# Optimization experiments

Hardware: AMD Instinct MI355X
Metric: run time of the kernel (lower is better)

Reference implementation:

```python
import math
import jax
import jax.numpy as jnp
import numpy as np

B = 64          # graphs per batch
NPG = 1000      # nodes per graph
IN = 64         # input feature dim
H = 128         # hidden dim
DEG = 16        # avg degree
C = 10          # num classes
RATIO = 0.8     # topk ratio
EPS = 1e-5      # batchnorm eps
E = B * NPG * DEG


def setup_inputs() -> dict:
    key = jax.random.key(0)
    ks = jax.random.split(key, 16)
    x = jax.random.normal(ks[0], (B * NPG, IN), jnp.float32)
    # per-graph random edges, then offset to global node ids
    src = jax.random.randint(ks[1], (B, NPG * DEG), 0, NPG)
    dst = jax.random.randint(ks[2], (B, NPG * DEG), 0, NPG)
    off = (jnp.arange(B) * NPG)[:, None]
    edge_index = jnp.stack([(src + off).reshape(-1), (dst + off).reshape(-1)]).astype(jnp.int32)
    batch = jnp.repeat(jnp.arange(B), NPG).astype(jnp.int32)
    edge_weight = jax.random.uniform(ks[3], (E,), jnp.float32)
    # parameters: block 1 conv is [IN,H]; blocks 2-6 are [H,H] (stacked)
    conv1_w = jax.random.normal(ks[4], (IN, H), jnp.float32) * 0.05
    conv_w = jax.random.normal(ks[5], (5, H, H), jnp.float32) * 0.05
    conv_b = jnp.zeros((6, H), jnp.float32)
    bn_gamma = jnp.ones((6, H), jnp.float32)
    bn_beta = jnp.zeros((6, H), jnp.float32)
    bn_mean = jax.random.normal(ks[6], (6, H), jnp.float32) * 0.01
    bn_var = jax.random.uniform(ks[7], (6, H), jnp.float32, 0.5, 1.5)
    pool_w = jax.random.normal(ks[8], (6, H), jnp.float32)
    d1_w = jax.random.normal(ks[9], (2 * H, 4 * H), jnp.float32) * 0.05
    d1_b = jnp.zeros((4 * H,), jnp.float32)
    d2_w = jax.random.normal(ks[10], (4 * H, C), jnp.float32) * 0.05
    d2_b = jnp.zeros((C,), jnp.float32)
    return dict(x=x, edge_index=edge_index, batch=batch, edge_weight=edge_weight,
                conv1_w=conv1_w, conv_w=conv_w, conv_b=conv_b,
                bn_gamma=bn_gamma, bn_beta=bn_beta, bn_mean=bn_mean, bn_var=bn_var,
                pool_w=pool_w, d1_w=d1_w, d1_b=d1_b, d2_w=d2_w, d2_b=d2_b)


def _gcn_conv(h, src, dst, w_e, W, b, n_nodes):
    # PyG GCNConv: add self-loops (weight 1), sym-normalize, aggregate at dst
    xw = h @ W                                        # [N, H]
    deg = jnp.zeros((n_nodes,), h.dtype).at[dst].add(w_e) + 1.0
    dinv = jax.lax.rsqrt(deg)
    coef = dinv[src] * dinv[dst] * w_e                # [E]
    out = jnp.zeros_like(xw).at[dst].add(coef[:, None] * xw[src])
    out = out + (dinv * dinv)[:, None] * xw + b       # self-loop term + bias
    return out


def reference(x, edge_index, batch, edge_weight, conv1_w, conv_w, conv_b,
              bn_gamma, bn_beta, bn_mean, bn_var, pool_w, d1_w, d1_b, d2_w, d2_b):
    src, dst = edge_index[0], edge_index[1]
    w_e = edge_weight
    h = x
    n_cur = NPG
    flats = jnp.zeros((B, 2 * H), x.dtype)
    for i in range(6):
        N = B * n_cur
        W = conv1_w if i == 0 else conv_w[i - 1]
        hc = _gcn_conv(h, src, dst, w_e, W, conv_b[i], N)
        # BatchNorm (inference) + ReLU
        hc = (hc - bn_mean[i]) * (bn_gamma[i] * jax.lax.rsqrt(bn_var[i] + EPS)) + bn_beta[i]
        hc = jax.nn.relu(hc)
        # TopKPooling: score = tanh(x.w/||w||), keep top ceil(ratio*n) per graph
        pw = pool_w[i]
        score = jnp.tanh(hc @ pw / jnp.linalg.norm(pw))   # [N]
        k = math.ceil(RATIO * n_cur)
        vals, idx = jax.lax.top_k(score.reshape(B, n_cur), k)  # [B,k]
        perm = (idx + (jnp.arange(B) * n_cur)[:, None]).reshape(-1)
        h = hc[perm] * vals.reshape(-1, 1)                # [B*k, H]
        # remap/filter edges; dead edges become (0,0) with weight 0
        inv = jnp.full((N,), -1, jnp.int32).at[perm].set(jnp.arange(B * k, dtype=jnp.int32))
        ok = (inv[src] >= 0) & (inv[dst] >= 0)
        src = jnp.where(ok, inv[src], 0)
        dst = jnp.where(ok, inv[dst], 0)
        w_e = jnp.where(ok, w_e, 0.0)
        n_cur = k
        hb = h.reshape(B, k, H)
        flats = flats + jnp.concatenate([hb.mean(axis=1), hb.max(axis=1)], axis=-1)
    # MLP head (dropout is identity in eval)
    hd = jax.nn.relu(flats @ d1_w + d1_b)
    return hd @ d2_w + d2_b
```

## Files before the change

### kernel.cpp

```cpp
#include <hip/hip_runtime.h>
#include <float.h>
#include <math.h>

#define NGR 64
#define NPG0 1000
#define HDIM 128
#define EG 16000
#define NE (NGR*EG)
#define RPS 1008
#define BNEPS 1e-5f
#define POOL_NB 16

typedef short short8 __attribute__((ext_vector_type(8)));
typedef float f4v __attribute__((ext_vector_type(4)));

__global__ __launch_bounds__(256) void k_wsplit(const float* __restrict__ c1w,
    const float* __restrict__ cw, const float* __restrict__ pw,
    unsigned short* __restrict__ wh, unsigned short* __restrict__ wl,
    float* __restrict__ invnorm){
  int l = blockIdx.x, t = threadIdx.x;
  __shared__ float red[2];
  if(t < 128){
    float v = pw[l*HDIM + t];
    float s = v*v;
    #pragma unroll
    for(int o=32;o>0;o>>=1) s += __shfl_down(s, o, 64);
    if((t & 63)==0) red[t>>6] = s;
  }
  __syncthreads();
  if(t==0) invnorm[l] = 1.0f / sqrtf(red[0]+red[1]);
  int K  = (l==0) ? 64 : 128;
  int sh = (l==0) ? 6 : 7;
  const float* src = (l==0) ? c1w : (cw + (size_t)(l-1)*16384);
  int tot = 128*K;
  for(int o=t;o<tot;o+=256){
    int c = o >> sh, k = o & (K-1);
    float f = src[k*128 + c];
    unsigned u  = __float_as_uint(f);
    unsigned uh = (u + 0x7fffu + ((u>>16)&1u)) & 0xffff0000u;
    float r = f - __uint_as_float(uh);
    unsigned v = __float_as_uint(r);
    int o2 = (k>>3)*1024 + c*8 + (k&7);
    wh[(size_t)l*16384 + o2] = (unsigned short)(uh>>16);
    wl[(size_t)l*16384 + o2] = (unsigned short)((v + 0x7fffu + ((v>>16)&1u))>>16);
  }
}

__global__ __launch_bounds__(256) void k_count0(const int* __restrict__ dst,
    const float* __restrict__ we, int* __restrict__ pcnt, float* __restrict__ pdeg){
  int g = blockIdx.x >> 2, sub = blockIdx.x & 3, t = threadIdx.x;
  __shared__ int   cnt[NPG0];
  __shared__ float degl[NPG0];
  for(int i=t;i<NPG0;i+=256){ cnt[i]=0; degl[i]=0.f; }
  __syncthreads();
  int base = g*EG + sub*4000;
  for(int idx=t; idx<4000; idx+=256){
    int e = base + idx;
    int ld = dst[e] - g*NPG0;
    atomicAdd(&cnt[ld], 1);
    atomicAdd(&degl[ld], we[e]);
  }
  __syncthreads();
  int p = blockIdx.x * NPG0;
  for(int i=t;i<NPG0;i+=256){ pcnt[p+i] = cnt[i]; pdeg[p+i] = degl[i]; }
}

__global__ __launch_bounds__(1024) void k_build(const int* __restrict__ pcnt,
    const float* __restrict__ pdeg, const int* __restrict__ src,
    const int* __restrict__ dst, const float* __restrict__ we,
    int* __restrict__ rp, float* __restrict__ dinvz, float* __restrict__ gsc,
    long long* __restrict__ ec){
  int g = blockIdx.x, t = threadIdx.x;
  __shared__ int sc[2][1024];
  __shared__ int cur[NPG0];
  int c = 0;
  if(t < NPG0){
    c = pcnt[(g*4+0)*NPG0+t] + pcnt[(g*4+1)*NPG0+t]
      + pcnt[(g*4+2)*NPG0+t] + pcnt[(g*4+3)*NPG0+t];
    float dg = pdeg[(g*4+0)*NPG0+t] + pdeg[(g*4+1)*NPG0+t]
             + pdeg[(g*4+2)*NPG0+t] + pdeg[(g*4+3)*NPG0+t];
    float dv = 1.0f / sqrtf(dg + 1.0f);
    dinvz[g*NPG0+t] = dv;
    gsc[g*NPG0+t]   = dv;
  }
  sc[0][t] = c;
  __syncthreads();
  int buf = 0;
  for(int d=1; d<1024; d<<=1){
    int v = sc[buf][t];
    if(t>=d) v += sc[buf][t-d];
    sc[buf^1][t] = v;
    __syncthreads();
    buf ^= 1;
  }
  if(t<=NPG0) rp[g*RPS+t] = (t==0) ? 0 : sc[buf][t-1];
  if(t<NPG0)  cur[t]      = (t==0) ? 0 : sc[buf][t-1];
  __syncthreads();
  int base = g*EG;
  for(int idx=t; idx<EG; idx+=1024){
    int e = base + idx;
    int ld = dst[e] - g*NPG0;
    int pos = atomicAdd(&cur[ld], 1);
    ec[(size_t)base + pos] = (((long long)__float_as_int(we[e]))<<32) | (unsigned)src[e];
  }
}

__device__ inline void bfsplit(float f, unsigned short &h, unsigned short &l){
  unsigned u  = __float_as_uint(f);
  unsigned uh = (u + 0x7fffu + ((u>>16)&1u)) & 0xffff0000u;
  float r = f - __uint_as_float(uh);
  unsigned v = __float_as_uint(r);
  h = (unsigned short)(uh>>16);
  l = (unsigned short)((v + 0x7fffu + ((v>>16)&1u))>>16);
}

template<int KIN>
__global__ __launch_bounds__(256) void k_fused(const int* __restrict__ olist,
    const int* __restrict__ rp, const long long* __restrict__ ec,
    const float* __restrict__ dinvz, const float* __restrict__ gsc,
    const float* __restrict__ h,
    const unsigned short* __restrict__ Wh, const unsigned short* __restrict__ Wl,
    const float* __restrict__ bias, const float* __restrict__ gamma,
    const float* __restrict__ beta, const float* __restrict__ mean,
    const float* __restrict__ var, const float* __restrict__ pw,
    const float* __restrict__ invn_p, float* __restrict__ hout,
    float* __restrict__ score){
  constexpr int L0 = (KIN==64);
  __shared__ __attribute__((aligned(16))) unsigned short AsH[32*KIN];
  __shared__ __attribute__((aligned(16))) unsigned short AsL[32*KIN];
  __shared__ float sp[32][2];
  int t = threadIdx.x;
  int nb = gridDim.x, b = blockIdx.x;
  int q = nb >> 3, r = nb & 7;
  int xcd = b & 7, off = b >> 3;
  int tile = (xcd < r) ? (xcd*(q+1) + off) : (r*(q+1) + (xcd-r)*q + off);
  int r0 = tile * 32;
  const int lane = t & 63, wid = t >> 6;
  const int wr = wid >> 1, wc = wid & 1;
  const int qw = lane >> 4, sl16 = lane & 15;

  for(int rr=0; rr<8; rr++){
    int local = wid*8 + rr;
    int row = r0 + local;
    int d = L0 ? row : olist[row];
    int g = d / NPG0;
    int ld = d - g*NPG0;
    int e0 = rp[g*RPS+ld], e1 = rp[g*RPS+ld+1];
    float dvd = dinvz[d];
    float gsd = gsc[d];
    float4 a0; a0.x=0.f; a0.y=0.f; a0.z=0.f; a0.w=0.f;
    float4 a1; a1.x=0.f; a1.y=0.f; a1.z=0.f; a1.w=0.f;
    for(int b2=e0;b2<e1;b2+=64){
      int mm = e1-b2; if(mm>64) mm=64;
      long long rec = (lane<mm) ? ec[(size_t)g*EG + b2 + lane] : 0;
      int   sl = (int)(rec & 0xffffffffLL);
      float cl = __int_as_float((int)(rec>>32)) * gsc[sl];
      long long pk = (((long long)__float_as_int(cl))<<32) | (unsigned)sl;
      int mr = (mm+15) & ~15;
      for(int jj=0;jj<mr;jj+=16){
        #pragma unroll
        for(int u=0;u<4;u++){
          long long p = __shfl(pk, jj + 4*u + qw, 64);
          float c = __int_as_float((int)(p>>32));
          if(c != 0.f){
            int s = (int)(p & 0xffffffffLL);
            if(L0){
              float4 hv = *(const float4*)(h + (size_t)s*64 + 4*sl16);
              a0.x += c*hv.x; a0.y += c*hv.y; a0.z += c*hv.z; a0.w += c*hv.w;
            } else {
              const float4* hp = (const float4*)(h + (size_t)s*HDIM + 8*sl16);
              float4 h0 = hp[0], h1 = hp[1];
              a0.x += c*h0.x; a0.y += c*h0.y; a0.z += c*h0.z; a0.w += c*h0.w;
              a1.x += c*h1.x; a1.y += c*h1.y; a1.z += c*h1.z; a1.w += c*h1.w;
            }
          }
        }
      }
    }
    a0.x += __shfl_xor(a0.x, 16, 64); a0.y += __shfl_xor(a0.y, 16, 64);
    a0.z += __shfl_xor(a0.z, 16, 64); a0.w += __shfl_xor(a0.w, 16, 64);
    a0.x += __shfl_xor(a0.x, 32, 64); a0.y += __shfl_xor(a0.y, 32, 64);
    a0.z += __shfl_xor(a0.z, 32, 64); a0.w += __shfl_xor(a0.w, 32, 64);
    if(!L0){
      a1.x += __shfl_xor(a1.x, 16, 64); a1.y += __shfl_xor(a1.y, 16, 64);
      a1.z += __shfl_xor(a1.z, 16, 64); a1.w += __shfl_xor(a1.w, 16, 64);
      a1.x += __shfl_xor(a1.x, 32, 64); a1.y += __shfl_xor(a1.y, 32, 64);
      a1.z += __shfl_xor(a1.z, 32, 64); a1.w += __shfl_xor(a1.w, 32, 64);
    }
    if(qw==0){
      if(L0){
        float4 hs = *(const float4*)(h + (size_t)d*64 + 4*sl16);
        float4 o;
        o.x = dvd*(a0.x + gsd*hs.x); o.y = dvd*(a0.y + gsd*hs.y);
        o.z = dvd*(a0.z + gsd*hs.z); o.w = dvd*(a0.w + gsd*hs.w);
        ushort4 h4, l4;
        bfsplit(o.x, h4.x, l4.x); bfsplit(o.y, h4.y, l4.y);
        bfsplit(o.z, h4.z, l4.z); bfsplit(o.w, h4.w, l4.w);
        int off2 = (local*128 + sl16*8) ^ ((local&7)<<4);
        *(ushort4*)((char*)AsH + off2) = h4;
        *(ushort4*)((char*)AsL + off2) = l4;
      } else {
        const float4* hp = (const float4*)(h + (size_t)d*HDIM + 8*sl16);
        float4 s0 = hp[0], s1 = hp[1];
        float4 o0, o1;
        o0.x = dvd*(a0.x + gsd*s0.x); o0.y = dvd*(a0.y + gsd*s0.y);
        o0.z = dvd*(a0.z + gsd*s0.z); o0.w = dvd*(a0.w + gsd*s0.w);
        o1.x = dvd*(a1.x + gsd*s1.x); o1.y = dvd*(a1.y + gsd*s1.y);
        o1.z = dvd*(a1.z + gsd*s1.z); o1.w = dvd*(a1.w + gsd*s1.w);
        ushort4 h4, l4;
        int off2 = (local*256 + sl16*16) ^ ((local&7)<<4);
        bfsplit(o0.x, h4.x, l4.x); bfsplit(o0.y, h4.y, l4.y);
        bfsplit(o0.z, h4.z, l4.z); bfsplit(o0.w, h4.w, l4.w);
        *(ushort4*)((char*)AsH + off2) = h4;
        *(ushort4*)((char*)AsL + off2) = l4;
        bfsplit(o1.x, h4.x, l4.x); bfsplit(o1.y, h4.y, l4.y);
        bfsplit(o1.z, h4.z, l4.z); bfsplit(o1.w, h4.w, l4.w);
        *(ushort4*)((char*)AsH + off2 + 8) = h4;
        *(ushort4*)((char*)AsL + off2 + 8) = l4;
      }
    }
  }
  __syncthreads();

  f4v acc[4];
  #pragma unroll
  for(int n=0;n<4;n++){ acc[n][0]=0.f; acc[n][1]=0.f; acc[n][2]=0.f; acc[n][3]=0.f; }
  #pragma unroll
  for(int ks=0; ks<KIN/32; ks++){
    short8 ah, al, bh[4], bl[4];
    int kb = ks*64 + qw*16;
    int panel = ks*4 + qw;
    #pragma unroll
    for(int n=0;n<4;n++){
      int col = wc*64 + n*16 + sl16;
      int goff = (panel*128 + col)*8;
      bh[n] = *(const short8*)(Wh + goff);
      bl[n] = *(const short8*)(Wl + goff);
    }
    {
      int row = wr*16 + sl16;
      int off2 = (row*(KIN*2) + kb) ^ ((row&7)<<4);
      ah = *(const short8*)((const char*)AsH + off2);
      al = *(const short8*)((const char*)AsL + off2);
    }
    #pragma unroll
    for(int n=0;n<4;n++){
      acc[n] = __builtin_amdgcn_mfma_f32_16x16x32_bf16(ah, bh[n], acc[n], 0,0,0);
      acc[n] = __builtin_amdgcn_mfma_f32_16x16x32_bf16(ah, bl[n], acc[n], 0,0,0);
      acc[n] = __builtin_amdgcn_mfma_f32_16x16x32_bf16(al, bh[n], acc[n], 0,0,0);
      acc[n] = __builtin_amdgcn_mfma_f32_16x16x32_bf16(al, bl[n], acc[n], 0,0,0);
    }
  }

  float invn = invn_p[0];
  float bi[4], scv[4], bt[4], mn[4], pv[4];
  #pragma unroll
  for(int n=0;n<4;n++){
    int c = wc*64 + n*16 + sl16;
    bi[n]  = bias[c];
    scv[n] = gamma[c] * (1.0f/sqrtf(var[c] + BNEPS));
    bt[n]  = beta[c];
    mn[n]  = mean[c];
    pv[n]  = pw[c];
  }
  #pragma unroll
  for(int i=0;i<4;i++){
    int rl  = wr*16 + qw*4 + i;
    int row = r0 + rl;
    int orig = olist ? olist[row] : row;
    float p = 0.f;
    #pragma unroll
    for(int n=0;n<4;n++){
      float v = fmaxf((acc[n][i] + bi[n] - mn[n])*scv[n] + bt[n], 0.f);
      hout[(size_t)orig*HDIM + wc*64 + n*16 + sl16] = v;
      p += v*pv[n];
    }
    p += __shfl_xor(p, 1, 64); p += __shfl_xor(p, 2, 64);
    p += __shfl_xor(p, 4, 64); p += __shfl_xor(p, 8, 64);
    if(sl16==0) sp[rl][wc] = p;
  }
  __syncthreads();
  if(t < 32) score[r0 + t] = tanhf((sp[t][0] + sp[t][1]) * invn);
}

__global__ __launch_bounds__(512) void k_topk(int n, int k,
    const float* __restrict__ score, const int* __restrict__ curlist,
    float* __restrict__ vals, int* __restrict__ nextlist,
    float* __restrict__ dinvz, float* __restrict__ gsc){
  int g = blockIdx.x, t = threadIdx.x;
  __shared__ unsigned keys[1024];
  __shared__ int hist[256];
  __shared__ int ssum[256];
  __shared__ int sc2[2][512];
  __shared__ int eqbuf[1024];
  __shared__ int eqn;
  __shared__ int sh_B, sh_need, sh_E, sh_cut;
  __shared__ unsigned sh_pref;
  for(int i=t;i<n;i+=512){
    unsigned b = __float_as_uint(score[g*n+i]);
    keys[i] = (b & 0x80000000u) ? ~b : (b | 0x80000000u);
  }
  if(t==0){ sh_need = k; sh_pref = 0u; sh_cut = 0x7fffffff; }
  __syncthreads();
  for(int pass=0; pass<4; pass++){
    int shift = 24 - 8*pass;
    if(t<256) hist[t]=0;
    __syncthreads();
    unsigned pref = sh_pref; int need = sh_need;
    for(int i=t;i<n;i+=512){
      unsigned u = keys[i];
      bool m = (pass==0) || ((u >> (shift+8)) == pref);
      if(m) atomicAdd(&hist[(u>>shift)&255], 1);
    }
    __syncthreads();
    if(t<256) ssum[t] = hist[t];
    __syncthreads();
    for(int d=1; d<256; d<<=1){
      int v=0;
      if(t<256) v = ssum[t] + ((t+d<256)? ssum[t+d] : 0);
      __syncthreads();
      if(t<256) ssum[t] = v;
      __syncthreads();
    }
    if(t<256){
      int Sgt = ssum[t] - hist[t];
      if(Sgt < need && need <= ssum[t]) sh_B = t;
    }
    __syncthreads();
    int B = sh_B;
    if(t==0){
      sh_need = need - (ssum[B] - hist[B]);
      sh_pref = (pass==0) ? (unsigned)B : ((pref<<8) | (unsigned)B);
      if(pass==3) sh_E = hist[B];
    }
    __syncthreads();
  }
  unsigned T = sh_pref; int r_eq = sh_need; int E = sh_E;
  if(E > r_eq){
    if(t==0) eqn = 0;
    __syncthreads();
    for(int i=t;i<n;i+=512) if(keys[i]==T){ int p=atomicAdd(&eqn,1); eqbuf[p]=i; }
    __syncthreads();
    if(t==0){
      int last = -1;
      for(int j=0;j<r_eq;j++){
        int mn = 0x7fffffff;
        for(int q=0;q<E;q++){ int v=eqbuf[q]; if(v>last && v<mn) mn=v; }
        last = mn;
      }
      sh_cut = last;
    }
    __syncthreads();
  }
  int cut = sh_cut;
  int c0=0, c1=0;
  {
    int i=t;
    if(i<n){ unsigned u=keys[i]; c0 = (u>T) || (u==T && i<=cut); }
    i=t+512;
    if(i<n){ unsigned u=keys[i]; c1 = (u>T) || (u==T && i<=cut); }
  }
  sc2[0][t] = c0+c1;
  __syncthreads();
  int buf=0;
  for(int d=1; d<512; d<<=1){
    int v = sc2[buf][t];
    if(t>=d) v += sc2[buf][t-d];
    sc2[buf^1][t]=v;
    __syncthreads();
    buf^=1;
  }
  int base = (t==0) ? 0 : sc2[buf][t-1];
  {
    int i=t;
    if(i<n){
      int orig = curlist ? curlist[g*n+i] : (g*NPG0 + i);
      if(c0){
        unsigned u=keys[i];
        float f = __uint_as_float((u & 0x80000000u) ? (u ^ 0x80000000u) : ~u);
        vals[g*k+base]=f; nextlist[g*k+base]=orig; base++;
      } else { dinvz[orig]=0.f; gsc[orig]=0.f; }
    }
    i=t+512;
    if(i<n){
      int orig = curlist ? curlist[g*n+i] : (g*NPG0 + i);
      if(c1){
        unsigned u=keys[i];
        float f = __uint_as_float((u & 0x80000000u) ? (u ^ 0x80000000u) : ~u);
        vals[g*k+base]=f; nextlist[g*k+base]=orig;
      } else { dinvz[orig]=0.f; gsc[orig]=0.f; }
    }
  }
}

__global__ __launch_bounds__(256) void k_gpd(int k, int do_deg,
    const float* __restrict__ hraw, const float* __restrict__ vals,
    const int* __restrict__ nextlist,
    float* __restrict__ sumst, float* __restrict__ maxst,
    const int* __restrict__ rp, const long long* __restrict__ ec,
    float* __restrict__ dinvz, float* __restrict__ gsc){
  int g = blockIdx.x & 63;
  int chunk = blockIdx.x >> 6;
  int wid = threadIdx.x >> 6, lane = threadIdx.x & 63;
  int ww = chunk*4 + wid;
  const int half = lane >> 5, sl32 = lane & 31;
  const int qw   = lane >> 4, sl16 = lane & 15;
  const int NH = POOL_NB*4*2;
  float4 psum; psum.x=0.f; psum.y=0.f; psum.z=0.f; psum.w=0.f;
  float4 pmax; pmax.x=-FLT_MAX; pmax.y=-FLT_MAX; pmax.z=-FLT_MAX; pmax.w=-FLT_MAX;
  for(int j = ww*2 + half; j < k; j += NH){
    float v = vals[g*k+j];
    int d = nextlist[g*k+j];
    float4 hv = *(const float4*)(hraw + (size_t)d*HDIM + 4*sl32);
    float4 o; o.x=hv.x*v; o.y=hv.y*v; o.z=hv.z*v; o.w=hv.w*v;
    psum.x+=o.x; psum.y+=o.y; psum.z+=o.z; psum.w+=o.w;
    pmax.x=fmaxf(pmax.x,o.x); pmax.y=fmaxf(pmax.y,o.y);
    pmax.z=fmaxf(pmax.z,o.z); pmax.w=fmaxf(pmax.w,o.w);
  }
  if(do_deg){
    const int NQ = POOL_NB*4*4;
    for(int j = ww*4 + qw; j < k; j += NQ){
      int d  = nextlist[g*k + j];
      int ld = d - g*NPG0;
      int e0 = rp[g*RPS+ld], e1 = rp[g*RPS+ld+1];
      float deg = 0.f;
      for(int b=e0+sl16; b<e1; b+=16){
        long long rec = ec[(size_t)g*EG + b];
        int s = (int)(rec & 0xffffffffLL);
        float w = __int_as_float((int)(rec>>32));
        if(dinvz[s] != 0.f) deg += w;
      }
      #pragma unroll
      for(int o=8;o>0;o>>=1) deg += __shfl_xor(deg, o, 64);
      if(sl16==0){
        float dv = 1.0f / sqrtf(deg + 1.0f);
        dinvz[d] = dv;
        gsc[d] = dv * vals[g*k+j];
      }
    }
  }
  psum.x += __shfl_xor(psum.x, 32, 64); psum.y += __shfl_xor(psum.y, 32, 64);
  psum.z += __shfl_xor(psum.z, 32, 64); psum.w += __shfl_xor(psum.w, 32, 64);
  pmax.x = fmaxf(pmax.x, __shfl_xor(pmax.x, 32, 64));
  pmax.y = fmaxf(pmax.y, __shfl_xor(pmax.y, 32, 64));
  pmax.z = fmaxf(pmax.z, __shfl_xor(pmax.z, 32, 64));
  pmax.w = fmaxf(pmax.w, __shfl_xor(pmax.w, 32, 64));
  __shared__ float ss[4][128];
  __shared__ float sm[4][128];
  if(half==0){
    *(float4*)&ss[wid][4*sl32] = psum;
    *(float4*)&sm[wid][4*sl32] = pmax;
  }
  __syncthreads();
  int t = threadIdx.x;
  if(t < 128){
    float s = (ss[0][t]+ss[1][t]) + (ss[2][t]+ss[3][t]);
    float m = fmaxf(fmaxf(sm[0][t], sm[1][t]), fmaxf(sm[2][t], sm[3][t]));
    sumst[(size_t)(chunk*NGR + g)*HDIM + t] = s;
    maxst[(size_t)(chunk*NGR + g)*HDIM + t] = m;
  }
}

__global__ __launch_bounds__(512) void k_head(const float* __restrict__ sumstage,
    const float* __restrict__ maxstage,
    const float* __restrict__ d1w, const float* __restrict__ d1b,
    const float* __restrict__ d2w, const float* __restrict__ d2b, float* __restrict__ out){
  const float kinv[6] = {1.f/800.f, 1.f/640.f, 1.f/512.f, 1.f/410.f, 1.f/328.f, 1.f/263.f};
  int g = blockIdx.x, j = threadIdx.x;
  __shared__ float fl[256];
  __shared__ float hd[512];
  if(j < 128){
    float s = 0.f;
    #pragma unroll
    for(int l=0;l<6;l++){
      float ls = 0.f;
      for(int c=0;c<POOL_NB;c++)
        ls += sumstage[(size_t)((l*POOL_NB + c)*NGR + g)*HDIM + j];
      s += ls * kinv[l];
    }
    fl[j] = s;
  } else if(j < 256){
    int f = j - 128;
    float m = 0.f;
    #pragma unroll
    for(int l=0;l<6;l++){
      float lm = -FLT_MAX;
      for(int c=0;c<POOL_NB;c++)
        lm = fmaxf(lm, maxstage[(size_t)((l*POOL_NB + c)*NGR + g)*HDIM + f]);
      m += lm;
    }
    fl[j] = m;
  }
  __syncthreads();
  float acc = d1b[j];
  for(int i=0;i<256;i++) acc += fl[i]*d1w[i*512+j];
  hd[j] = fmaxf(acc, 0.f);
  __syncthreads();
  if(j < 10){
    float a = d2b[j];
    for(int i=0;i<512;i++) a += hd[i]*d2w[i*10+j];
    out[g*10+j] = a;
  }
}

extern "C" void kernel_launch(void* const* d_in, const int* in_sizes, int n_in,
                              void* d_out, int out_size, void* d_ws, size_t ws_size,
                              hipStream_t stream) {
  const float* x    = (const float*)d_in[0];
  const int* ei     = (const int*)d_in[1];
  const float* ew   = (const float*)d_in[3];
  const float* conv1w = (const float*)d_in[4];
  const float* convw  = (const float*)d_in[5];
  const float* convb  = (const float*)d_in[6];
  const float* bng    = (const float*)d_in[7];
  const float* bnb    = (const float*)d_in[8];
  const float* bnm    = (const float*)d_in[9];
  const float* bnv    = (const float*)d_in[10];
  const float* poolw  = (const float*)d_in[11];
  const float* d1w    = (const float*)d_in[12];
  const float* d1b    = (const float*)d_in[13];
  const float* d2w    = (const float*)d_in[14];
  const float* d2b    = (const float*)d_in[15];
  float* out = (float*)d_out;

  char* w = (char*)d_ws;
  float* hbufA = (float*)w; w += (size_t)64000*128*4;
  float* hbufB = (float*)w; w += (size_t)64000*128*4;
  long long* ec = (long long*)w; w += (size_t)NE*8;
  int*   rp    = (int*)w;   w += (size_t)NGR*RPS*4;
  int*   pcnt  = (int*)w;   w += (size_t)256*NPG0*4;
  float* pdeg  = (float*)w; w += (size_t)256*NPG0*4;
  float* dinvz = (float*)w; w += (size_t)64000*4;
  float* gsc   = (float*)w; w += (size_t)64000*4;
  float* score = (float*)w; w += (size_t)64000*4;
  float* vals  = (float*)w; w += (size_t)51200*4;
  int*   listA = (int*)w;   w += (size_t)51200*4;
  int*   listB = (int*)w;   w += (size_t)51200*4;
  float* invno = (float*)w; w += 64;
  float* sumstage = (float*)w; w += (size_t)6*POOL_NB*NGR*HDIM*4;
  float* maxstage = (float*)w; w += (size_t)6*POOL_NB*NGR*HDIM*4;
  unsigned short* whi = (unsigned short*)w; w += (size_t)6*16384*2;
  unsigned short* wlo = (unsigned short*)w; w += (size_t)6*16384*2;

  k_wsplit<<<6,256,0,stream>>>(conv1w, convw, poolw, whi, wlo, invno);

  const int ns[6]={1000,800,640,512,410,328};
  const int ks[6]={800,640,512,410,328,263};

  k_count0<<<256,256,0,stream>>>(ei+NE, ew, pcnt, pdeg);
  k_build<<<64,1024,0,stream>>>(pcnt, pdeg, ei, ei+NE, ew, rp, dinvz, gsc, ec);

  k_fused<64><<<2000,256,0,stream>>>(nullptr, rp, ec, dinvz, gsc, x, whi, wlo,
                                     convb, bng, bnb, bnm, bnv, poolw, invno,
                                     hbufA, score);
  k_topk<<<64,512,0,stream>>>(1000, 800, score, nullptr, vals, listA, dinvz, gsc);
  k_gpd<<<64*POOL_NB,256,0,stream>>>(800, 1, hbufA, vals, listA,
                                     sumstage, maxstage, rp, ec, dinvz, gsc);

  int* cur = listA; int* nxt = listB;
  float* hin = hbufA; float* hot = hbufB;
  for(int i=1;i<6;i++){
    int n = ns[i], k = ks[i];
    k_fused<128><<<2*n,256,0,stream>>>(cur, rp, ec, dinvz, gsc, hin,
                                       whi + (size_t)i*16384, wlo + (size_t)i*16384,
                                       convb+i*128, bng+i*128, bnb+i*128, bnm+i*128,
                                       bnv+i*128, poolw+i*128, invno+i,
                                       hot, score);
    k_topk<<<64,512,0,stream>>>(n, k, score, cur, vals, nxt, dinvz, gsc);
    k_gpd<<<64*POOL_NB,256,0,stream>>>(k, (i<5)?1:0, hot, vals, nxt,
                                       sumstage + (size_t)i*POOL_NB*NGR*HDIM,
                                       maxstage + (size_t)i*POOL_NB*NGR*HDIM,
                                       rp, ec, dinvz, gsc);
    int* tmp = cur; cur = nxt; nxt = tmp;
    float* htmp = hin; hin = hot; hot = htmp;
  }

  k_head<<<64,512,0,stream>>>(sumstage, maxstage, d1w, d1b, d2w, d2b, out);
}
```

Baseline: 521.7 us.

## Halve fused GCN tile to 16 rows, one row per quarter-wave gather

The fused aggregate+GEMM kernel now processes 16 rows per block instead of 32, with each 16-lane quarter-wave gathering one destination row independently, so the cross-quarter shuffle reductions go away. Grid size doubles, and each wave computes a 16x32 output slice instead of 16x64. This is meant to improve load balance and latency hiding in the irregular edge gather and to drop the reduction shuffles. In exchange, weight fragments are reloaded by twice as many blocks, and each quarter-wave now walks its edges serially, so unbalanced degrees within a wave leave lanes idle.

```diff
diff --git a/kernel.cpp b/kernel.cpp
--- a/kernel.cpp
+++ b/kernel.cpp
@@ -126,21 +126,20 @@
     const float* __restrict__ invn_p, float* __restrict__ hout,
     float* __restrict__ score){
   constexpr int L0 = (KIN==64);
-  __shared__ __attribute__((aligned(16))) unsigned short AsH[32*KIN];
-  __shared__ __attribute__((aligned(16))) unsigned short AsL[32*KIN];
-  __shared__ float sp[32][2];
+  __shared__ __attribute__((aligned(16))) unsigned short AsH[16*KIN];
+  __shared__ __attribute__((aligned(16))) unsigned short AsL[16*KIN];
+  __shared__ float sp[16][4];
   int t = threadIdx.x;
   int nb = gridDim.x, b = blockIdx.x;
   int q = nb >> 3, r = nb & 7;
-  int xcd = b & 7, off = b >> 3;
-  int tile = (xcd < r) ? (xcd*(q+1) + off) : (r*(q+1) + (xcd-r)*q + off);
-  int r0 = tile * 32;
+  int xcd = b & 7, boff = b >> 3;
+  int tile = (xcd < r) ? (xcd*(q+1) + boff) : (r*(q+1) + (xcd-r)*q + boff);
+  int r0 = tile * 16;
   const int lane = t & 63, wid = t >> 6;
-  const int wr = wid >> 1, wc = wid & 1;
   const int qw = lane >> 4, sl16 = lane & 15;
 
-  for(int rr=0; rr<8; rr++){
-    int local = wid*8 + rr;
+  {
+    int local = wid*4 + qw;
     int row = r0 + local;
     int d = L0 ? row : olist[row];
     int g = d / NPG0;
@@ -150,101 +149,85 @@
     float gsd = gsc[d];
     float4 a0; a0.x=0.f; a0.y=0.f; a0.z=0.f; a0.w=0.f;
     float4 a1; a1.x=0.f; a1.y=0.f; a1.z=0.f; a1.w=0.f;
-    for(int b2=e0;b2<e1;b2+=64){
-      int mm = e1-b2; if(mm>64) mm=64;
-      long long rec = (lane<mm) ? ec[(size_t)g*EG + b2 + lane] : 0;
+    for(int b2=e0;b2<e1;b2+=16){
+      int mm = e1-b2; if(mm>16) mm=16;
+      long long rec = (sl16<mm) ? ec[(size_t)g*EG + b2 + sl16] : 0;
       int   sl = (int)(rec & 0xffffffffLL);
       float cl = __int_as_float((int)(rec>>32)) * gsc[sl];
       long long pk = (((long long)__float_as_int(cl))<<32) | (unsigned)sl;
-      int mr = (mm+15) & ~15;
-      for(int jj=0;jj<mr;jj+=16){
-        #pragma unroll
-        for(int u=0;u<4;u++){
-          long long p = __shfl(pk, jj + 4*u + qw, 64);
-          float c = __int_as_float((int)(p>>32));
-          if(c != 0.f){
-            int s = (int)(p & 0xffffffffLL);
-            if(L0){
-              float4 hv = *(const float4*)(h + (size_t)s*64 + 4*sl16);
-              a0.x += c*hv.x; a0.y += c*hv.y; a0.z += c*hv.z; a0.w += c*hv.w;
-            } else {
-              const float4* hp = (const float4*)(h + (size_t)s*HDIM + 8*sl16);
-              float4 h0 = hp[0], h1 = hp[1];
-              a0.x += c*h0.x; a0.y += c*h0.y; a0.z += c*h0.z; a0.w += c*h0.w;
-              a1.x += c*h1.x; a1.y += c*h1.y; a1.z += c*h1.z; a1.w += c*h1.w;
-            }
+      for(int jj=0;jj<mm;jj++){
+        long long p = __shfl(pk, (qw<<4) + jj, 64);
+        float c = __int_as_float((int)(p>>32));
+        if(c != 0.f){
+          int s = (int)(p & 0xffffffffLL);
+          if(L0){
+            float4 hv = *(const float4*)(h + (size_t)s*64 + 4*sl16);
+            a0.x += c*hv.x; a0.y += c*hv.y; a0.z += c*hv.z; a0.w += c*hv.w;
+          } else {
+            const float4* hp = (const float4*)(h + (size_t)s*HDIM + 8*sl16);
+            float4 h0 = hp[0], h1 = hp[1];
+            a0.x += c*h0.x; a0.y += c*h0.y; a0.z += c*h0.z; a0.w += c*h0.w;
+            a1.x += c*h1.x; a1.y += c*h1.y; a1.z += c*h1.z; a1.w += c*h1.w;
           }
         }
       }
     }
-    a0.x += __shfl_xor(a0.x, 16, 64); a0.y += __shfl_xor(a0.y, 16, 64);
-    a0.z += __shfl_xor(a0.z, 16, 64); a0.w += __shfl_xor(a0.w, 16, 64);
-    a0.x += __shfl_xor(a0.x, 32, 64); a0.y += __shfl_xor(a0.y, 32, 64);
-    a0.z += __shfl_xor(a0.z, 32, 64); a0.w += __shfl_xor(a0.w, 32, 64);
-    if(!L0){
-      a1.x += __shfl_xor(a1.x, 16, 64); a1.y += __shfl_xor(a1.y, 16, 64);
-      a1.z += __shfl_xor(a1.z, 16, 64); a1.w += __shfl_xor(a1.w, 16, 64);
-      a1.x += __shfl_xor(a1.x, 32, 64); a1.y += __shfl_xor(a1.y, 32, 64);
-      a1.z += __shfl_xor(a1.z, 32, 64); a1.w += __shfl_xor(a1.w, 32, 64);
-    }
-    if(qw==0){
-      if(L0){
-        float4 hs = *(const float4*)(h + (size_t)d*64 + 4*sl16);
-        float4 o;
-        o.x = dvd*(a0.x + gsd*hs.x); o.y = dvd*(a0.y + gsd*hs.y);
-        o.z = dvd*(a0.z + gsd*hs.z); o.w = dvd*(a0.w + gsd*hs.w);
-        ushort4 h4, l4;
-        bfsplit(o.x, h4.x, l4.x); bfsplit(o.y, h4.y, l4.y);
-        bfsplit(o.z, h4.z, l4.z); bfsplit(o.w, h4.w, l4.w);
-        int off2 = (local*128 + sl16*8) ^ ((local&7)<<4);
-        *(ushort4*)((char*)AsH + off2) = h4;
-        *(ushort4*)((char*)AsL + off2) = l4;
-      } else {
-        const float4* hp = (const float4*)(h + (size_t)d*HDIM + 8*sl16);
-        float4 s0 = hp[0], s1 = hp[1];
-        float4 o0, o1;
-        o0.x = dvd*(a0.x + gsd*s0.x); o0.y = dvd*(a0.y + gsd*s0.y);
-        o0.z = dvd*(a0.z + gsd*s0.z); o0.w = dvd*(a0.w + gsd*s0.w);
-        o1.x = dvd*(a1.x + gsd*s1.x); o1.y = dvd*(a1.y + gsd*s1.y);
-        o1.z = dvd*(a1.z + gsd*s1.z); o1.w = dvd*(a1.w + gsd*s1.w);
-        ushort4 h4, l4;
-        int off2 = (local*256 + sl16*16) ^ ((local&7)<<4);
-        bfsplit(o0.x, h4.x, l4.x); bfsplit(o0.y, h4.y, l4.y);
-        bfsplit(o0.z, h4.z, l4.z); bfsplit(o0.w, h4.w, l4.w);
-        *(ushort4*)((char*)AsH + off2) = h4;
-        *(ushort4*)((char*)AsL + off2) = l4;
-        bfsplit(o1.x, h4.x, l4.x); bfsplit(o1.y, h4.y, l4.y);
-        bfsplit(o1.z, h4.z, l4.z); bfsplit(o1.w, h4.w, l4.w);
-        *(ushort4*)((char*)AsH + off2 + 8) = h4;
-        *(ushort4*)((char*)AsL + off2 + 8) = l4;
-      }
-    }
-  }
-  __syncthreads();
-
-  f4v acc[4];
+    if(L0){
+      float4 hs = *(const float4*)(h + (size_t)d*64 + 4*sl16);
+      float4 o;
+      o.x = dvd*(a0.x + gsd*hs.x); o.y = dvd*(a0.y + gsd*hs.y);
+      o.z = dvd*(a0.z + gsd*hs.z); o.w = dvd*(a0.w + gsd*hs.w);
+      ushort4 h4, l4;
+      bfsplit(o.x, h4.x, l4.x); bfsplit(o.y, h4.y, l4.y);
+      bfsplit(o.z, h4.z, l4.z); bfsplit(o.w, h4.w, l4.w);
+      int off2 = (local*128 + sl16*8) ^ ((local&7)<<4);
+      *(ushort4*)((char*)AsH + off2) = h4;
+      *(ushort4*)((char*)AsL + off2) = l4;
+    } else {
+      const float4* hp = (const float4*)(h + (size_t)d*HDIM + 8*sl16);
+      float4 s0 = hp[0], s1 = hp[1];
+      float4 o0, o1;
+      o0.x = dvd*(a0.x + gsd*s0.x); o0.y = dvd*(a0.y + gsd*s0.y);
+      o0.z = dvd*(a0.z + gsd*s0.z); o0.w = dvd*(a0.w + gsd*s0.w);
+      o1.x = dvd*(a1.x + gsd*s1.x); o1.y = dvd*(a1.y + gsd*s1.y);
+      o1.z = dvd*(a1.z + gsd*s1.z); o1.w = dvd*(a1.w + gsd*s1.w);
+      ushort4 h4, l4;
+      int off2 = (local*256 + sl16*16) ^ ((local&7)<<4);
+      bfsplit(o0.x, h4.x, l4.x); bfsplit(o0.y, h4.y, l4.y);
+      bfsplit(o0.z, h4.z, l4.z); bfsplit(o0.w, h4.w, l4.w);
+      *(ushort4*)((char*)AsH + off2) = h4;
+      *(ushort4*)((char*)AsL + off2) = l4;
+      bfsplit(o1.x, h4.x, l4.x); bfsplit(o1.y, h4.y, l4.y);
+      bfsplit(o1.z, h4.z, l4.z); bfsplit(o1.w, h4.w, l4.w);
+      *(ushort4*)((char*)AsH + off2 + 8) = h4;
+      *(ushort4*)((char*)AsL + off2 + 8) = l4;
+    }
+  }
+  __syncthreads();
+
+  f4v acc[2];
   #pragma unroll
-  for(int n=0;n<4;n++){ acc[n][0]=0.f; acc[n][1]=0.f; acc[n][2]=0.f; acc[n][3]=0.f; }
+  for(int n=0;n<2;n++){ acc[n][0]=0.f; acc[n][1]=0.f; acc[n][2]=0.f; acc[n][3]=0.f; }
   #pragma unroll
   for(int ks=0; ks<KIN/32; ks++){
-    short8 ah, al, bh[4], bl[4];
+    short8 ah, al, bh[2], bl[2];
     int kb = ks*64 + qw*16;
     int panel = ks*4 + qw;
     #pragma unroll
-    for(int n=0;n<4;n++){
-      int col = wc*64 + n*16 + sl16;
+    for(int n=0;n<2;n++){
+      int col = wid*32 + n*16 + sl16;
       int goff = (panel*128 + col)*8;
       bh[n] = *(const short8*)(Wh + goff);
       bl[n] = *(const short8*)(Wl + goff);
     }
     {
-      int row = wr*16 + sl16;
+      int row = sl16;
       int off2 = (row*(KIN*2) + kb) ^ ((row&7)<<4);
       ah = *(const short8*)((const char*)AsH + off2);
       al = *(const short8*)((const char*)AsL + off2);
     }
     #pragma unroll
-    for(int n=0;n<4;n++){
+    for(int n=0;n<2;n++){
       acc[n] = __builtin_amdgcn_mfma_f32_16x16x32_bf16(ah, bh[n], acc[n], 0,0,0);
       acc[n] = __builtin_amdgcn_mfma_f32_16x16x32_bf16(ah, bl[n], acc[n], 0,0,0);
       acc[n] = __builtin_amdgcn_mfma_f32_16x16x32_bf16(al, bh[n], acc[n], 0,0,0);
@@ -253,10 +236,10 @@
   }
 
   float invn = invn_p[0];
-  float bi[4], scv[4], bt[4], mn[4], pv[4];
+  float bi[2], scv[2], bt[2], mn[2], pv[2];
   #pragma unroll
-  for(int n=0;n<4;n++){
-    int c = wc*64 + n*16 + sl16;
+  for(int n=0;n<2;n++){
+    int c = wid*32 + n*16 + sl16;
     bi[n]  = bias[c];
     scv[n] = gamma[c] * (1.0f/sqrtf(var[c] + BNEPS));
     bt[n]  = beta[c];
@@ -265,22 +248,22 @@
   }
   #pragma unroll
   for(int i=0;i<4;i++){
-    int rl  = wr*16 + qw*4 + i;
+    int rl  = qw*4 + i;
     int row = r0 + rl;
     int orig = olist ? olist[row] : row;
     float p = 0.f;
     #pragma unroll
-    for(int n=0;n<4;n++){
+    for(int n=0;n<2;n++){
       float v = fmaxf((acc[n][i] + bi[n] - mn[n])*scv[n] + bt[n], 0.f);
-      hout[(size_t)orig*HDIM + wc*64 + n*16 + sl16] = v;
+      hout[(size_t)orig*HDIM + wid*32 + n*16 + sl16] = v;
       p += v*pv[n];
     }
     p += __shfl_xor(p, 1, 64); p += __shfl_xor(p, 2, 64);
     p += __shfl_xor(p, 4, 64); p += __shfl_xor(p, 8, 64);
-    if(sl16==0) sp[rl][wc] = p;
-  }
-  __syncthreads();
-  if(t < 32) score[r0 + t] = tanhf((sp[t][0] + sp[t][1]) * invn);
+    if(sl16==0) sp[rl][wid] = p;
+  }
+  __syncthreads();
+  if(t < 16) score[r0 + t] = tanhf(((sp[t][0]+sp[t][1]) + (sp[t][2]+sp[t][3])) * invn);
 }
 
 __global__ __launch_bounds__(512) void k_topk(int n, int k,
@@ -550,7 +533,7 @@
   k_count0<<<256,256,0,stream>>>(ei+NE, ew, pcnt, pdeg);
   k_build<<<64,1024,0,stream>>>(pcnt, pdeg, ei, ei+NE, ew, rp, dinvz, gsc, ec);
 
-  k_fused<64><<<2000,256,0,stream>>>(nullptr, rp, ec, dinvz, gsc, x, whi, wlo,
+  k_fused<64><<<4000,256,0,stream>>>(nullptr, rp, ec, dinvz, gsc, x, whi, wlo,
                                      convb, bng, bnb, bnm, bnv, poolw, invno,
                                      hbufA, score);
   k_topk<<<64,512,0,stream>>>(1000, 800, score, nullptr, vals, listA, dinvz, gsc);
@@ -561,7 +544,7 @@
   float* hin = hbufA; float* hot = hbufB;
   for(int i=1;i<6;i++){
     int n = ns[i], k = ks[i];
-    k_fused<128><<<2*n,256,0,stream>>>(cur, rp, ec, dinvz, gsc, hin,
+    k_fused<128><<<4*n,256,0,stream>>>(cur, rp, ec, dinvz, gsc, hin,
                                        whi + (size_t)i*16384, wlo + (size_t)i*16384,
                                        convb+i*128, bng+i*128, bnb+i*128, bnm+i*128,
                                        bnv+i*128, poolw+i*128, invno+i,
```

After: 424.0 us. 18.7% less time.
